# Kernel tuning notes

Hardware: AMD Instinct MI355X
Metric: run time of the kernel (lower is better)

## Reference

```python
import jax, jax.numpy as jnp
import numpy as np

PADDING_L = 15  # init arg padding_l

def setup_inputs() -> dict:
    key = jax.random.key(0)
    k1, k2 = jax.random.split(key)
    T, B, C = 2048, 2, 1024
    H, K = 16, 31
    x = jax.random.normal(k1, (T, B, C), dtype=jnp.float32)
    # xavier-uniform-ish init for (H, 1, K)
    limit = float(np.sqrt(6.0 / (1 + K)))
    weight = jax.random.uniform(k2, (H, 1, K), dtype=jnp.float32, minval=-limit, maxval=limit)
    return {"x": x, "weight": weight}


def reference(x, weight):
    T, B, C = x.shape
    H, _, K = weight.shape
    R = C // H
    P = PADDING_L
    # softmax-normalized per-head kernel weights (weight_softmax path)
    w = jax.nn.softmax(weight.reshape(H, K), axis=1)  # (H, K)

    # --- output: depthwise 'same' conv, out[t] = sum_k w[k] * x[t - P + k] ---
    kern = jnp.repeat(w, R, axis=0)[:, None, :]       # (C, 1, K)
    xb = jnp.transpose(x, (1, 2, 0))                   # (B, C, T)
    out = jax.lax.conv_general_dilated(
        xb, kern, window_strides=(1,), padding=[(P, K - 1 - P)],
        dimension_numbers=("NCH", "OIH", "NCH"), feature_group_count=C)
    output = jnp.transpose(out, (2, 0, 1))             # (T, B, C)

    # --- weight_expanded: banded Toeplitz matrix, returned by the module ---
    t = jnp.arange(T)
    off = t[None, :] - t[:, None] + P                  # (T, T), band offset
    valid = (off >= 0) & (off < K)
    band = jnp.where(valid, w[:, jnp.clip(off, 0, K - 1)], 0.0)  # (H, T, T)
    weight_expanded = jnp.broadcast_to(band[None], (B, H, T, T)).reshape(B * H, T, T)

    return output, weight_expanded
```

## Files before the change

### kernel.cpp

```cpp
#include <hip/hip_runtime.h>

#define T_DIM 2048
#define B_DIM 2
#define C_DIM 1024
#define H_DIM 16
#define K_DIM 31
#define P_PAD 15
#define BC    (B_DIM * C_DIM)
#define TT    32

#define CONV_BLOCKS 512
#define GRID_BLKS   2560
#define N4_TOTAL    33554432u
#define SWEEP_STRIDE (GRID_BLKS * 256u)
#define SWEEP_ITERS  52

typedef float v4f __attribute__((ext_vector_type(4)));

__global__ __launch_bounds__(256) void k_fused(const float* __restrict__ x,
                                               const float* __restrict__ w,
                                               float* __restrict__ out,
                                               float* __restrict__ we) {
    __shared__ float lw[H_DIM * K_DIM];
    const int tid = threadIdx.x;

    if (tid < H_DIM) {
        float v[K_DIM];
        float m = -1e30f;
#pragma unroll
        for (int k = 0; k < K_DIM; ++k) { v[k] = w[tid * K_DIM + k]; m = fmaxf(m, v[k]); }
        float s = 0.f;
#pragma unroll
        for (int k = 0; k < K_DIM; ++k) { v[k] = expf(v[k] - m); s += v[k]; }
        float inv = 1.f / s;
#pragma unroll
        for (int k = 0; k < K_DIM; ++k) lw[tid * K_DIM + k] = v[k] * inv;
    }
    __syncthreads();

    const int bid = blockIdx.x;

    if (bid < CONV_BLOCKS) {
        const int colBase = (bid & 7) * 256;
        const int t0      = (bid >> 3) * TT;
        const int col     = colBase + tid;
        const int h       = (col & (C_DIM - 1)) >> 6;

        float wr[K_DIM];
#pragma unroll
        for (int k = 0; k < K_DIM; ++k) wr[k] = lw[h * K_DIM + k];

        float xv[TT + K_DIM - 1];
#pragma unroll
        for (int r = 0; r < TT + K_DIM - 1; ++r) {
            int t = t0 - P_PAD + r;
            xv[r] = (t >= 0 && t < T_DIM) ? x[t * BC + col] : 0.f;
        }
#pragma unroll
        for (int i = 0; i < TT; ++i) {
            float acc = 0.f;
#pragma unroll
            for (int k = 0; k < K_DIM; ++k) acc = fmaf(wr[k], xv[i + k], acc);
            out[(t0 + i) * BC + col] = acc;
        }
    }

    unsigned pos = (unsigned)bid + 2048u;
    if (pos >= GRID_BLKS) pos -= GRID_BLKS;
    const unsigned fbase = pos * 256u + (unsigned)tid;

    v4f* we4 = (v4f*)we;
#pragma unroll 4
    for (unsigned it = 0; it < SWEEP_ITERS; ++it) {
        const unsigned f = it * SWEEP_STRIDE + fbase;
        if (f < N4_TOTAL) {
            const unsigned bh  = f >> 20;
            const unsigned rem = f & 0xFFFFFu;
            const unsigned i   = rem >> 9;
            const int      j4  = (int)((rem & 511u) << 2);
            const int      d   = j4 - (int)i + P_PAD;

            v4f v = (v4f)0.f;
            if (d > -4 && d < K_DIM) {
                const float* wrow = lw + (bh & (H_DIM - 1)) * K_DIM;
                v.x = (d     >= 0 && d     < K_DIM) ? wrow[d]     : 0.f;
                v.y = (d + 1 >= 0 && d + 1 < K_DIM) ? wrow[d + 1] : 0.f;
                v.z = (d + 2 >= 0 && d + 2 < K_DIM) ? wrow[d + 2] : 0.f;
                v.w = (d + 3 >= 0 && d + 3 < K_DIM) ? wrow[d + 3] : 0.f;
            }
            we4[f] = v;
        }
    }
}

extern "C" void kernel_launch(void* const* d_in, const int* in_sizes, int n_in,
                              void* d_out, int out_size, void* d_ws, size_t ws_size,
                              hipStream_t stream) {
    const float* x = (const float*)d_in[0];
    const float* w = (const float*)d_in[1];
    float* out = (float*)d_out;
    float* we  = out + (size_t)T_DIM * B_DIM * C_DIM;

    k_fused<<<GRID_BLKS, 256, 0, stream>>>(x, w, out, we);
}
```

Measured before the change: 111.2 us.

## Split grid into dedicated conv blocks and dedicated Toeplitz sweep blocks

Replaces the design in which every block joined the weight_expanded sweep after the optional conv work with a split grid. The first 512 blocks now run only the conv and 256 separate blocks run only the Toeplitz fill, each looping 512 iterations with no bounds check. This drops the total block count and the per-iteration bounds branch, and simplifies the index math. The risk is load imbalance: the 256 sweep blocks may not saturate write bandwidth, and the conv blocks no longer help with the large store stream.

```diff
diff --git a/kernel.cpp b/kernel.cpp
--- a/kernel.cpp
+++ b/kernel.cpp
@@ -9,11 +9,12 @@
 #define BC    (B_DIM * C_DIM)
 #define TT    32
 
-#define CONV_BLOCKS 512
-#define GRID_BLKS   2560
-#define N4_TOTAL    33554432u
-#define SWEEP_STRIDE (GRID_BLKS * 256u)
-#define SWEEP_ITERS  52
+#define CONV_BLOCKS  512
+#define SWEEP_BLOCKS 256
+#define GRID_BLKS    (CONV_BLOCKS + SWEEP_BLOCKS)
+#define N4_TOTAL     33554432u
+#define SWEEP_STRIDE (SWEEP_BLOCKS * 256u)
+#define SWEEP_ITERS  (N4_TOTAL / SWEEP_STRIDE)
 
 typedef float v4f __attribute__((ext_vector_type(4)));
 
@@ -63,30 +64,23 @@
             for (int k = 0; k < K_DIM; ++k) acc = fmaf(wr[k], xv[i + k], acc);
             out[(t0 + i) * BC + col] = acc;
         }
-    }
-
-    unsigned pos = (unsigned)bid + 2048u;
-    if (pos >= GRID_BLKS) pos -= GRID_BLKS;
-    const unsigned fbase = pos * 256u + (unsigned)tid;
-
-    v4f* we4 = (v4f*)we;
+    } else {
+        const unsigned f0 = (unsigned)(bid - CONV_BLOCKS) * 256u + (unsigned)tid;
+        v4f* we4 = (v4f*)we;
 #pragma unroll 4
-    for (unsigned it = 0; it < SWEEP_ITERS; ++it) {
-        const unsigned f = it * SWEEP_STRIDE + fbase;
-        if (f < N4_TOTAL) {
-            const unsigned bh  = f >> 20;
-            const unsigned rem = f & 0xFFFFFu;
-            const unsigned i   = rem >> 9;
-            const int      j4  = (int)((rem & 511u) << 2);
-            const int      d   = j4 - (int)i + P_PAD;
+        for (unsigned it = 0; it < SWEEP_ITERS; ++it) {
+            const unsigned f   = it * SWEEP_STRIDE + f0;
+            const unsigned row = f >> 9;
+            const int      i   = (int)(row & (T_DIM - 1));
+            const int      d0  = (int)((f & 511u) << 2) - i + P_PAD;
 
             v4f v = (v4f)0.f;
-            if (d > -4 && d < K_DIM) {
-                const float* wrow = lw + (bh & (H_DIM - 1)) * K_DIM;
-                v.x = (d     >= 0 && d     < K_DIM) ? wrow[d]     : 0.f;
-                v.y = (d + 1 >= 0 && d + 1 < K_DIM) ? wrow[d + 1] : 0.f;
-                v.z = (d + 2 >= 0 && d + 2 < K_DIM) ? wrow[d + 2] : 0.f;
-                v.w = (d + 3 >= 0 && d + 3 < K_DIM) ? wrow[d + 3] : 0.f;
+            if (d0 >= -3 && d0 <= 30) {
+                const float* wrow = lw + ((row >> 11) & (H_DIM - 1)) * K_DIM;
+                v.x = (d0     >= 0) ? wrow[d0]     : 0.f;
+                v.y = (d0 + 1 >= 0 && d0 + 1 < K_DIM) ? wrow[d0 + 1] : 0.f;
+                v.z = (d0 + 2 >= 0 && d0 + 2 < K_DIM) ? wrow[d0 + 2] : 0.f;
+                v.w = (d0 + 3 >= 0 && d0 + 3 < K_DIM) ? wrow[d0 + 3] : 0.f;
             }
             we4[f] = v;
         }
```

Result: faster. 107.9 us (-3.0%).
